# Optimization experiments

Hardware: AMD Instinct MI355X
Metric: run time of the kernel (lower is better)

The kernel has to match this reference:

```python
import jax, jax.numpy as jnp
import numpy as np

D = 256
NR_PATHS, PATH_LEN = 4096, 64
NR_NODES = 10000


def setup_inputs() -> dict:
    key = jax.random.key(0)
    ks = jax.random.split(key, 6)
    encoded_paths = jax.random.normal(ks[0], (NR_PATHS, PATH_LEN, D), dtype=jnp.float32)
    paths_mask = jax.random.randint(ks[1], (NR_PATHS, PATH_LEN), 0, 2).astype(jnp.bool_)
    paths_node_indices = jax.random.randint(ks[2], (NR_PATHS, PATH_LEN), 0, NR_NODES)
    previous_nodes_encodings = jax.random.normal(ks[3], (NR_NODES, D), dtype=jnp.float32)
    Wq = jax.random.normal(ks[4], (D, D), dtype=jnp.float32) / np.sqrt(D)
    gate_W = jax.random.normal(ks[5], (2 * D, D), dtype=jnp.float32) / np.sqrt(2 * D)
    gate_b = jnp.zeros((D,), dtype=jnp.float32)
    return {
        'encoded_paths': encoded_paths,
        'paths_mask': paths_mask,
        'paths_node_indices': paths_node_indices,
        'previous_nodes_encodings': previous_nodes_encodings,
        'Wq': Wq,
        'gate_W': gate_W,
        'gate_b': gate_b,
        'nr_nodes': NR_NODES,
    }


def _scatter_attn_combine(x, idx, m, queries, Wq, nr_nodes):
    # x: [N, D] flattened path-step encodings; idx: [N] target node; m: [N] bool mask
    d = x.shape[-1]
    q = queries @ Wq                                   # [nodes, D] attention queries
    scores = jnp.einsum('nd,nd->n', q[idx], x) / jnp.sqrt(jnp.asarray(d, x.dtype))
    scores = jnp.where(m, scores, jnp.asarray(-1e30, x.dtype))
    seg_max = jax.ops.segment_max(scores, idx, num_segments=nr_nodes)
    seg_max = jnp.where(jnp.isfinite(seg_max), seg_max, jnp.zeros_like(seg_max))
    e = jnp.exp(scores - seg_max[idx]) * m.astype(x.dtype)
    denom = jax.ops.segment_sum(e, idx, num_segments=nr_nodes)
    probs = e / jnp.maximum(denom[idx], jnp.asarray(1e-9, x.dtype))
    return jax.ops.segment_sum(probs[:, None] * x, idx, num_segments=nr_nodes)


def reference(encoded_paths, paths_mask, paths_node_indices,
              previous_nodes_encodings, Wq, gate_W, gate_b, nr_nodes):
    d = encoded_paths.shape[-1]
    x = encoded_paths.reshape(-1, d)
    idx = paths_node_indices.reshape(-1)
    m = paths_mask.reshape(-1)
    # attention-weighted scatter of masked path-step encodings onto nodes
    update = _scatter_attn_combine(x, idx, m, previous_nodes_encodings, Wq, nr_nodes)
    # gated state update: g = sigmoid([prev; update] W + b); new = g*prev + (1-g)*update
    g = jax.nn.sigmoid(jnp.concatenate([previous_nodes_encodings, update], axis=-1) @ gate_W + gate_b)
    return g * previous_nodes_encodings + (1.0 - g) * update
```

## Files before the change

kernel.cpp:

```cpp
#include <hip/hip_runtime.h>

#define D 256
#define NPATHS 4096
#define PLEN 64
#define NSTEPS (NPATHS * PLEN)
#define NNODES 10000

__global__ __launch_bounds__(256) void k_query(const float* __restrict__ prev,
                                               const float* __restrict__ Wq,
                                               float* __restrict__ q) {
    __shared__ float a[32][D];
    const int tid = threadIdx.x;
    const int row0 = blockIdx.x * 32;
    for (int i = tid; i < 32 * D; i += 256) {
        int r = i >> 8, c = i & 255;
        int row = row0 + r;
        a[r][c] = (row < NNODES) ? prev[row * D + c] : 0.f;
    }
    __syncthreads();
    float acc[32];
#pragma unroll
    for (int r = 0; r < 32; ++r) acc[r] = 0.f;
    for (int k = 0; k < D; k += 4) {
        float w0 = Wq[(k + 0) * D + tid];
        float w1 = Wq[(k + 1) * D + tid];
        float w2 = Wq[(k + 2) * D + tid];
        float w3 = Wq[(k + 3) * D + tid];
#pragma unroll
        for (int r = 0; r < 32; ++r) {
            float4 av = *reinterpret_cast<const float4*>(&a[r][k]);
            acc[r] += av.x * w0 + av.y * w1 + av.z * w2 + av.w * w3;
        }
    }
    for (int r = 0; r < 32; ++r) {
        int row = row0 + r;
        if (row < NNODES) q[row * D + tid] = acc[r];
    }
}

__global__ __launch_bounds__(256) void k_count(const int* __restrict__ mask,
                                               const int* __restrict__ nidx,
                                               int* __restrict__ counts) {
    const int step = blockIdx.x * 256 + threadIdx.x;
    if (step >= NSTEPS) return;
    if (!mask[step]) return;
    atomicAdd(&counts[nidx[step]], 1);
}

__global__ __launch_bounds__(256) void k_scan(const int* __restrict__ counts,
                                              int* __restrict__ offsets,
                                              int* __restrict__ cursor) {
    __shared__ int sums[256];
    __shared__ int scan[257];
    const int tid = threadIdx.x;
    const int CH = 40;
    const int base = tid * CH;
    int s = 0;
    for (int i = 0; i < CH; ++i) {
        int j = base + i;
        if (j < NNODES) s += counts[j];
    }
    sums[tid] = s;
    __syncthreads();
    if (tid == 0) {
        int run = 0;
        for (int t = 0; t < 256; ++t) { scan[t] = run; run += sums[t]; }
        scan[256] = run;
    }
    __syncthreads();
    int run = scan[tid];
    for (int i = 0; i < CH; ++i) {
        int j = base + i;
        if (j < NNODES) {
            offsets[j] = run;
            cursor[j] = run;
            run += counts[j];
        }
    }
    if (tid == 0) offsets[NNODES] = scan[256];
}

__global__ __launch_bounds__(256) void k_perm(const int* __restrict__ mask,
                                              const int* __restrict__ nidx,
                                              int* __restrict__ cursor,
                                              int* __restrict__ perm) {
    const int step = blockIdx.x * 256 + threadIdx.x;
    if (step >= NSTEPS) return;
    if (!mask[step]) return;
    const int node = nidx[step];
    int p = atomicAdd(&cursor[node], 1);
    perm[p] = step;
}

__global__ __launch_bounds__(256) void k_combine(const float* __restrict__ x,
                                                 const float* __restrict__ q,
                                                 const int* __restrict__ offsets,
                                                 const int* __restrict__ perm,
                                                 float* __restrict__ update) {
    const int wave = threadIdx.x >> 6;
    const int lane = threadIdx.x & 63;
    const int node = blockIdx.x * 4 + wave;
    if (node >= NNODES) return;
    const int off = offsets[node];
    const int cnt = offsets[node + 1] - off;

    const float4* x4 = reinterpret_cast<const float4*>(x);
    float4 qa = reinterpret_cast<const float4*>(q)[(size_t)node * 64 + lane];

    float4 acc = make_float4(0.f, 0.f, 0.f, 0.f);
    float m = -3.0e38f;
    float l = 0.f;

    int step = (cnt > 0) ? perm[off] : 0;
    float4 xa = (cnt > 0) ? x4[(size_t)step * 64 + lane]
                          : make_float4(0.f, 0.f, 0.f, 0.f);

    for (int i = 0; i < cnt; ++i) {
        int step_n = 0;
        if (i + 1 < cnt) step_n = perm[off + i + 1];
        float4 xn = make_float4(0.f, 0.f, 0.f, 0.f);
        if (i + 1 < cnt) xn = x4[(size_t)step_n * 64 + lane];

        float s = xa.x * qa.x + xa.y * qa.y + xa.z * qa.z + xa.w * qa.w;
        s += __shfl_xor(s, 32);
        s += __shfl_xor(s, 16);
        s += __shfl_xor(s, 8);
        s += __shfl_xor(s, 4);
        s += __shfl_xor(s, 2);
        s += __shfl_xor(s, 1);
        s *= 0.0625f;

        float mn = fmaxf(m, s);
        float scale = __expf(m - mn);
        float w = __expf(s - mn);
        l = l * scale + w;
        acc.x = acc.x * scale + w * xa.x;
        acc.y = acc.y * scale + w * xa.y;
        acc.z = acc.z * scale + w * xa.z;
        acc.w = acc.w * scale + w * xa.w;
        m = mn;

        xa = xn;
    }

    const float inv = 1.f / fmaxf(l, 1e-9f);
    float4 o = make_float4(acc.x * inv, acc.y * inv, acc.z * inv, acc.w * inv);
    reinterpret_cast<float4*>(update)[(size_t)node * 64 + lane] = o;
}

__global__ __launch_bounds__(256) void k_gate(const float* __restrict__ prev,
                                              const float* __restrict__ update,
                                              const float* __restrict__ gW,
                                              const float* __restrict__ gb,
                                              float* __restrict__ out) {
    __shared__ float pa[16][D];
    __shared__ float ua[16][D];
    const int tid = threadIdx.x;
    const int row0 = blockIdx.x * 16;
    for (int i = tid; i < 16 * D; i += 256) {
        int r = i >> 8, c = i & 255;
        int row = row0 + r;
        pa[r][c] = (row < NNODES) ? prev[row * D + c] : 0.f;
        ua[r][c] = (row < NNODES) ? update[row * D + c] : 0.f;
    }
    __syncthreads();
    float acc[16];
#pragma unroll
    for (int r = 0; r < 16; ++r) acc[r] = 0.f;
    for (int k = 0; k < D; k += 4) {
        float w0 = gW[(k + 0) * D + tid];
        float w1 = gW[(k + 1) * D + tid];
        float w2 = gW[(k + 2) * D + tid];
        float w3 = gW[(k + 3) * D + tid];
#pragma unroll
        for (int r = 0; r < 16; ++r) {
            float4 av = *reinterpret_cast<const float4*>(&pa[r][k]);
            acc[r] += av.x * w0 + av.y * w1 + av.z * w2 + av.w * w3;
        }
    }
    for (int k = 0; k < D; k += 4) {
        float w0 = gW[(256 + k + 0) * D + tid];
        float w1 = gW[(256 + k + 1) * D + tid];
        float w2 = gW[(256 + k + 2) * D + tid];
        float w3 = gW[(256 + k + 3) * D + tid];
#pragma unroll
        for (int r = 0; r < 16; ++r) {
            float4 av = *reinterpret_cast<const float4*>(&ua[r][k]);
            acc[r] += av.x * w0 + av.y * w1 + av.z * w2 + av.w * w3;
        }
    }
    const float b = gb[tid];
    for (int r = 0; r < 16; ++r) {
        int row = row0 + r;
        if (row < NNODES) {
            float g = 1.f / (1.f + expf(-(acc[r] + b)));
            out[row * D + tid] = g * pa[r][tid] + (1.f - g) * ua[r][tid];
        }
    }
}

extern "C" void kernel_launch(void* const* d_in, const int* in_sizes, int n_in,
                              void* d_out, int out_size, void* d_ws, size_t ws_size,
                              hipStream_t stream) {
    const float* enc   = (const float*)d_in[0];
    const int*   mask  = (const int*)d_in[1];
    const int*   nidx  = (const int*)d_in[2];
    const float* prev  = (const float*)d_in[3];
    const float* Wq    = (const float*)d_in[4];
    const float* gW    = (const float*)d_in[5];
    const float* gb    = (const float*)d_in[6];
    float* out = (float*)d_out;

    char* ws = (char*)d_ws;
    float* q       = (float*)(ws + 0);
    int*   counts  = (int*)  (ws + 10240000);
    int*   offsets = (int*)  (ws + 10280192);
    int*   cursor  = (int*)  (ws + 10320640);
    int*   perm    = (int*)  (ws + 10360832);
    float* update  = (float*)(ws + 11409408);

    hipMemsetAsync(counts, 0, NNODES * sizeof(int), stream);

    k_query<<<(NNODES + 31) / 32, 256, 0, stream>>>(prev, Wq, q);
    k_count<<<NSTEPS / 256, 256, 0, stream>>>(mask, nidx, counts);
    k_scan<<<1, 256, 0, stream>>>(counts, offsets, cursor);
    k_perm<<<NSTEPS / 256, 256, 0, stream>>>(mask, nidx, cursor, perm);
    k_combine<<<(NNODES + 3) / 4, 256, 0, stream>>>(enc, q, offsets, perm, update);
    k_gate<<<(NNODES + 15) / 16, 256, 0, stream>>>(prev, update, gW, gb, out);
}
```

Measured before the change: 584.9 us.

## Rework query/gate GEMVs to single-wave float4 tiles, shuffle scan, batched perm loads

The query and gate matmuls become single-wave blocks in which each lane computes four output columns for eight rows. Rows are read directly from global memory instead of being staged in shared memory. The scan replaces its serial single-thread pass with a wave shuffle prefix sum. The combine kernel loads 64 permutation indices per wave at once and keeps a two-deep x prefetch, which takes the dependent perm load off the critical path. The risk is that the new GEMV blocks may get lower occupancy or poorer weight reuse, and that per-lane reads of prev rows may be less coalesced.

```diff
diff --git a/kernel.cpp b/kernel.cpp
--- a/kernel.cpp
+++ b/kernel.cpp
@@ -6,36 +6,38 @@
 #define NSTEPS (NPATHS * PLEN)
 #define NNODES 10000
 
-__global__ __launch_bounds__(256) void k_query(const float* __restrict__ prev,
-                                               const float* __restrict__ Wq,
-                                               float* __restrict__ q) {
-    __shared__ float a[32][D];
-    const int tid = threadIdx.x;
-    const int row0 = blockIdx.x * 32;
-    for (int i = tid; i < 32 * D; i += 256) {
-        int r = i >> 8, c = i & 255;
-        int row = row0 + r;
-        a[r][c] = (row < NNODES) ? prev[row * D + c] : 0.f;
-    }
-    __syncthreads();
-    float acc[32];
-#pragma unroll
-    for (int r = 0; r < 32; ++r) acc[r] = 0.f;
-    for (int k = 0; k < D; k += 4) {
-        float w0 = Wq[(k + 0) * D + tid];
-        float w1 = Wq[(k + 1) * D + tid];
-        float w2 = Wq[(k + 2) * D + tid];
-        float w3 = Wq[(k + 3) * D + tid];
-#pragma unroll
-        for (int r = 0; r < 32; ++r) {
-            float4 av = *reinterpret_cast<const float4*>(&a[r][k]);
-            acc[r] += av.x * w0 + av.y * w1 + av.z * w2 + av.w * w3;
-        }
-    }
-    for (int r = 0; r < 32; ++r) {
-        int row = row0 + r;
-        if (row < NNODES) q[row * D + tid] = acc[r];
-    }
+__device__ __forceinline__ void fma4(float4& acc, float s, const float4& w) {
+    acc.x += s * w.x; acc.y += s * w.y; acc.z += s * w.z; acc.w += s * w.w;
+}
+
+#define QR 8
+__global__ __launch_bounds__(64) void k_query(const float* __restrict__ prev,
+                                              const float* __restrict__ Wq,
+                                              float* __restrict__ q) {
+    const int lane = threadIdx.x;
+    const int row0 = blockIdx.x * QR;
+    const float4* W4 = reinterpret_cast<const float4*>(Wq);
+    float4 acc[QR];
+#pragma unroll
+    for (int r = 0; r < QR; ++r) acc[r] = make_float4(0.f, 0.f, 0.f, 0.f);
+
+    for (int k4 = 0; k4 < 64; ++k4) {
+        float4 w0 = W4[(k4 * 4 + 0) * 64 + lane];
+        float4 w1 = W4[(k4 * 4 + 1) * 64 + lane];
+        float4 w2 = W4[(k4 * 4 + 2) * 64 + lane];
+        float4 w3 = W4[(k4 * 4 + 3) * 64 + lane];
+#pragma unroll
+        for (int r = 0; r < QR; ++r) {
+            float4 a = *reinterpret_cast<const float4*>(&prev[(size_t)(row0 + r) * D + k4 * 4]);
+            fma4(acc[r], a.x, w0);
+            fma4(acc[r], a.y, w1);
+            fma4(acc[r], a.z, w2);
+            fma4(acc[r], a.w, w3);
+        }
+    }
+    float4* Q4 = reinterpret_cast<float4*>(q);
+#pragma unroll
+    for (int r = 0; r < QR; ++r) Q4[(size_t)(row0 + r) * 64 + lane] = acc[r];
 }
 
 __global__ __launch_bounds__(256) void k_count(const int* __restrict__ mask,
@@ -50,9 +52,9 @@
 __global__ __launch_bounds__(256) void k_scan(const int* __restrict__ counts,
                                               int* __restrict__ offsets,
                                               int* __restrict__ cursor) {
-    __shared__ int sums[256];
-    __shared__ int scan[257];
     const int tid = threadIdx.x;
+    const int lane = tid & 63;
+    const int w = tid >> 6;
     const int CH = 40;
     const int base = tid * CH;
     int s = 0;
@@ -60,15 +62,17 @@
         int j = base + i;
         if (j < NNODES) s += counts[j];
     }
-    sums[tid] = s;
+    int v = s;
+    for (int d = 1; d < 64; d <<= 1) {
+        int t = __shfl_up(v, d);
+        if (lane >= d) v += t;
+    }
+    __shared__ int wsum[4];
+    if (lane == 63) wsum[w] = v;
     __syncthreads();
-    if (tid == 0) {
-        int run = 0;
-        for (int t = 0; t < 256; ++t) { scan[t] = run; run += sums[t]; }
-        scan[256] = run;
-    }
-    __syncthreads();
-    int run = scan[tid];
+    int woff = 0;
+    for (int i = 0; i < w; ++i) woff += wsum[i];
+    int run = woff + v - s;
     for (int i = 0; i < CH; ++i) {
         int j = base + i;
         if (j < NNODES) {
@@ -77,7 +81,7 @@
             run += counts[j];
         }
     }
-    if (tid == 0) offsets[NNODES] = scan[256];
+    if (tid == 255) offsets[NNODES] = run;
 }
 
 __global__ __launch_bounds__(256) void k_perm(const int* __restrict__ mask,
@@ -111,36 +115,45 @@
     float m = -3.0e38f;
     float l = 0.f;
 
-    int step = (cnt > 0) ? perm[off] : 0;
-    float4 xa = (cnt > 0) ? x4[(size_t)step * 64 + lane]
-                          : make_float4(0.f, 0.f, 0.f, 0.f);
-
-    for (int i = 0; i < cnt; ++i) {
-        int step_n = 0;
-        if (i + 1 < cnt) step_n = perm[off + i + 1];
-        float4 xn = make_float4(0.f, 0.f, 0.f, 0.f);
-        if (i + 1 < cnt) xn = x4[(size_t)step_n * 64 + lane];
-
-        float s = xa.x * qa.x + xa.y * qa.y + xa.z * qa.z + xa.w * qa.w;
-        s += __shfl_xor(s, 32);
-        s += __shfl_xor(s, 16);
-        s += __shfl_xor(s, 8);
-        s += __shfl_xor(s, 4);
-        s += __shfl_xor(s, 2);
-        s += __shfl_xor(s, 1);
-        s *= 0.0625f;
-
-        float mn = fmaxf(m, s);
-        float scale = __expf(m - mn);
-        float w = __expf(s - mn);
-        l = l * scale + w;
-        acc.x = acc.x * scale + w * xa.x;
-        acc.y = acc.y * scale + w * xa.y;
-        acc.z = acc.z * scale + w * xa.z;
-        acc.w = acc.w * scale + w * xa.w;
-        m = mn;
-
-        xa = xn;
+    for (int base = 0; base < cnt; base += 64) {
+        const int lim = min(64, cnt - base);
+        int myperm = perm[off + base + lane];
+
+        float4 xs0, xs1;
+        {
+            int s0 = __shfl(myperm, 0);
+            xs0 = x4[(size_t)s0 * 64 + lane];
+        }
+        if (lim > 1) {
+            int s1 = __shfl(myperm, 1);
+            xs1 = x4[(size_t)s1 * 64 + lane];
+        }
+        for (int i = 0; i < lim; ++i) {
+            float4 cur = (i & 1) ? xs1 : xs0;
+            if (i + 2 < lim) {
+                int sn = __shfl(myperm, i + 2);
+                float4 xn = x4[(size_t)sn * 64 + lane];
+                if (i & 1) xs1 = xn; else xs0 = xn;
+            }
+            float s = cur.x * qa.x + cur.y * qa.y + cur.z * qa.z + cur.w * qa.w;
+            s += __shfl_xor(s, 32);
+            s += __shfl_xor(s, 16);
+            s += __shfl_xor(s, 8);
+            s += __shfl_xor(s, 4);
+            s += __shfl_xor(s, 2);
+            s += __shfl_xor(s, 1);
+            s *= 0.0625f;
+
+            float mn = fmaxf(m, s);
+            float scale = __expf(m - mn);
+            float wgt = __expf(s - mn);
+            l = l * scale + wgt;
+            acc.x = acc.x * scale + wgt * cur.x;
+            acc.y = acc.y * scale + wgt * cur.y;
+            acc.z = acc.z * scale + wgt * cur.z;
+            acc.w = acc.w * scale + wgt * cur.w;
+            m = mn;
+        }
     }
 
     const float inv = 1.f / fmaxf(l, 1e-9f);
@@ -148,54 +161,66 @@
     reinterpret_cast<float4*>(update)[(size_t)node * 64 + lane] = o;
 }
 
-__global__ __launch_bounds__(256) void k_gate(const float* __restrict__ prev,
-                                              const float* __restrict__ update,
-                                              const float* __restrict__ gW,
-                                              const float* __restrict__ gb,
-                                              float* __restrict__ out) {
-    __shared__ float pa[16][D];
-    __shared__ float ua[16][D];
-    const int tid = threadIdx.x;
-    const int row0 = blockIdx.x * 16;
-    for (int i = tid; i < 16 * D; i += 256) {
-        int r = i >> 8, c = i & 255;
-        int row = row0 + r;
-        pa[r][c] = (row < NNODES) ? prev[row * D + c] : 0.f;
-        ua[r][c] = (row < NNODES) ? update[row * D + c] : 0.f;
-    }
-    __syncthreads();
-    float acc[16];
-#pragma unroll
-    for (int r = 0; r < 16; ++r) acc[r] = 0.f;
-    for (int k = 0; k < D; k += 4) {
-        float w0 = gW[(k + 0) * D + tid];
-        float w1 = gW[(k + 1) * D + tid];
-        float w2 = gW[(k + 2) * D + tid];
-        float w3 = gW[(k + 3) * D + tid];
-#pragma unroll
-        for (int r = 0; r < 16; ++r) {
-            float4 av = *reinterpret_cast<const float4*>(&pa[r][k]);
-            acc[r] += av.x * w0 + av.y * w1 + av.z * w2 + av.w * w3;
-        }
-    }
-    for (int k = 0; k < D; k += 4) {
-        float w0 = gW[(256 + k + 0) * D + tid];
-        float w1 = gW[(256 + k + 1) * D + tid];
-        float w2 = gW[(256 + k + 2) * D + tid];
-        float w3 = gW[(256 + k + 3) * D + tid];
-#pragma unroll
-        for (int r = 0; r < 16; ++r) {
-            float4 av = *reinterpret_cast<const float4*>(&ua[r][k]);
-            acc[r] += av.x * w0 + av.y * w1 + av.z * w2 + av.w * w3;
-        }
-    }
-    const float b = gb[tid];
-    for (int r = 0; r < 16; ++r) {
-        int row = row0 + r;
-        if (row < NNODES) {
-            float g = 1.f / (1.f + expf(-(acc[r] + b)));
-            out[row * D + tid] = g * pa[r][tid] + (1.f - g) * ua[r][tid];
-        }
+#define GR 8
+__global__ __launch_bounds__(64) void k_gate(const float* __restrict__ prev,
+                                             const float* __restrict__ update,
+                                             const float* __restrict__ gW,
+                                             const float* __restrict__ gb,
+                                             float* __restrict__ out) {
+    const int lane = threadIdx.x;
+    const int row0 = blockIdx.x * GR;
+    const float4* W4 = reinterpret_cast<const float4*>(gW);
+    float4 acc[GR];
+#pragma unroll
+    for (int r = 0; r < GR; ++r) acc[r] = make_float4(0.f, 0.f, 0.f, 0.f);
+
+    for (int k4 = 0; k4 < 64; ++k4) {
+        float4 w0 = W4[(k4 * 4 + 0) * 64 + lane];
+        float4 w1 = W4[(k4 * 4 + 1) * 64 + lane];
+        float4 w2 = W4[(k4 * 4 + 2) * 64 + lane];
+        float4 w3 = W4[(k4 * 4 + 3) * 64 + lane];
+#pragma unroll
+        for (int r = 0; r < GR; ++r) {
+            float4 a = *reinterpret_cast<const float4*>(&prev[(size_t)(row0 + r) * D + k4 * 4]);
+            fma4(acc[r], a.x, w0);
+            fma4(acc[r], a.y, w1);
+            fma4(acc[r], a.z, w2);
+            fma4(acc[r], a.w, w3);
+        }
+    }
+    for (int k4 = 0; k4 < 64; ++k4) {
+        float4 w0 = W4[(256 + k4 * 4 + 0) * 64 + lane];
+        float4 w1 = W4[(256 + k4 * 4 + 1) * 64 + lane];
+        float4 w2 = W4[(256 + k4 * 4 + 2) * 64 + lane];
+        float4 w3 = W4[(256 + k4 * 4 + 3) * 64 + lane];
+#pragma unroll
+        for (int r = 0; r < GR; ++r) {
+            float4 a = *reinterpret_cast<const float4*>(&update[(size_t)(row0 + r) * D + k4 * 4]);
+            fma4(acc[r], a.x, w0);
+            fma4(acc[r], a.y, w1);
+            fma4(acc[r], a.z, w2);
+            fma4(acc[r], a.w, w3);
+        }
+    }
+    const float4* P4 = reinterpret_cast<const float4*>(prev);
+    const float4* U4 = reinterpret_cast<const float4*>(update);
+    const float4 b4 = reinterpret_cast<const float4*>(gb)[lane];
+    float4* O4 = reinterpret_cast<float4*>(out);
+#pragma unroll
+    for (int r = 0; r < GR; ++r) {
+        const size_t ri = (size_t)(row0 + r) * 64 + lane;
+        float4 p = P4[ri];
+        float4 u = U4[ri];
+        float gx = 1.f / (1.f + __expf(-(acc[r].x + b4.x)));
+        float gy = 1.f / (1.f + __expf(-(acc[r].y + b4.y)));
+        float gz = 1.f / (1.f + __expf(-(acc[r].z + b4.z)));
+        float gw = 1.f / (1.f + __expf(-(acc[r].w + b4.w)));
+        float4 o;
+        o.x = gx * p.x + (1.f - gx) * u.x;
+        o.y = gy * p.y + (1.f - gy) * u.y;
+        o.z = gz * p.z + (1.f - gz) * u.z;
+        o.w = gw * p.w + (1.f - gw) * u.w;
+        O4[ri] = o;
     }
 }
 
@@ -221,10 +246,10 @@
 
     hipMemsetAsync(counts, 0, NNODES * sizeof(int), stream);
 
-    k_query<<<(NNODES + 31) / 32, 256, 0, stream>>>(prev, Wq, q);
+    k_query<<<NNODES / QR, 64, 0, stream>>>(prev, Wq, q);
     k_count<<<NSTEPS / 256, 256, 0, stream>>>(mask, nidx, counts);
     k_scan<<<1, 256, 0, stream>>>(counts, offsets, cursor);
     k_perm<<<NSTEPS / 256, 256, 0, stream>>>(mask, nidx, cursor, perm);
     k_combine<<<(NNODES + 3) / 4, 256, 0, stream>>>(enc, q, offsets, perm, update);
-    k_gate<<<(NNODES + 15) / 16, 256, 0, stream>>>(prev, update, gW, gb, out);
-}
+    k_gate<<<NNODES / GR, 64, 0, stream>>>(prev, update, gW, gb, out);
+}
```

Result: faster. 535.5 us (-8.4%).
